# Kernel tuning notes

Measured on AMD Instinct MI355X. Metric: run time of the kernel, lower is better.

Reference implementation:

```python
import jax, jax.numpy as jnp
import numpy as np

B, L, H, C = 1, 512, 1024, 2


def setup_inputs() -> dict:
    key = jax.random.key(0)
    k1, k2, k3 = jax.random.split(key, 3)
    lm_output = jax.random.normal(k1, (B, L, H), dtype=jnp.float32)
    # torch Linear weight layout: [out_features, in_features]
    W1 = jax.random.normal(k2, (H, 2 * H), dtype=jnp.float32) * 0.02
    b1 = jnp.zeros((H,), dtype=jnp.float32)
    W2 = jax.random.normal(k3, (C, H), dtype=jnp.float32) * 0.02
    b2 = jnp.zeros((C,), dtype=jnp.float32)
    return {"lm_output": lm_output, "W1": W1, "b1": b1, "W2": W2, "b2": b2}


def reference(lm_output, W1, b1, W2, b2):
    # pair_emb[b,i,j] = concat(lm_output[b,j], lm_output[b,i])
    # Linear(concat(a,b)) decomposes: split W1 into the halves acting on each part.
    Wa = W1[:, :H]  # acts on lm_output_a (the j / column token)
    Wb = W1[:, H:]  # acts on lm_output_b (the i / row token)
    a_proj = jnp.einsum('blh,oh->blo', lm_output, Wa)  # [B,L,H]
    b_proj = jnp.einsum('blh,oh->blo', lm_output, Wb)  # [B,L,H]
    # hidden[b,i,j] = tanh(a_proj[b,j] + b_proj[b,i] + b1)   -> [B,L,L,H]
    hidden = jnp.tanh(a_proj[:, None, :, :] + b_proj[:, :, None, :] + b1)
    # Dropout is identity at inference time.
    logits = jnp.einsum('bijh,ch->bijc', hidden, W2) + b2  # [B,L,L,C]
    logits = (logits + jnp.swapaxes(logits, 1, 2)) / 2.0
    return logits
```

## Files before the change

kernel.cpp:

```cpp
#include <hip/hip_runtime.h>
#include <hip/hip_bf16.h>

#define HH 1024
#define LL 512
#define NT 16
#define NTRI 136

typedef __attribute__((ext_vector_type(8))) short bf16x8;
typedef __attribute__((ext_vector_type(4))) float f32x4;
typedef __attribute__((ext_vector_type(2))) float f32x2;

static constexpr float C_EXP = 2.8853900817779268f;

static __device__ __forceinline__ uint4 pack8(float4 a, float4 b) {
    union { uint4 u; __hip_bfloat162 h[4]; } r;
    r.h[0] = __float22bfloat162_rn(make_float2(a.x, a.y));
    r.h[1] = __float22bfloat162_rn(make_float2(a.z, a.w));
    r.h[2] = __float22bfloat162_rn(make_float2(b.x, b.y));
    r.h[3] = __float22bfloat162_rn(make_float2(b.z, b.w));
    return r.u;
}

__global__ __launch_bounds__(256) void convert_kernel(
    const float* __restrict__ lm, const float* __restrict__ W1,
    const float* __restrict__ W2,
    ushort* __restrict__ lm16, ushort* __restrict__ B16, float* __restrict__ wsum)
{
    const int b = blockIdx.x;
    if (b == 1280) {
        const int tid = threadIdx.x;
        if (tid < 128) {
            const int c = tid >> 6, l = tid & 63;
            float s = 0.f;
            for (int q = l; q < 256; q += 64) {
                const float4 v = *(const float4*)&W2[c * HH + q * 4];
                s += v.x + v.y + v.z + v.w;
            }
#pragma unroll
            for (int off = 32; off; off >>= 1) s += __shfl_down(s, off, 64);
            if (l == 0) wsum[c] = s;
        }
        return;
    }
    const int q = b * 256 + threadIdx.x;
    if (q < 65536) {
        const float4 a = *(const float4*)&lm[q * 8];
        const float4 c = *(const float4*)&lm[q * 8 + 4];
        ((uint4*)lm16)[q] = pack8(a, c);
    } else {
        const int p = q - 65536;
        const int n = p >> 7, k8 = (p & 127) * 8;
        const float* src = &W1[(n & 1023) * 2048 + (n >> 10) * 1024 + k8];
        ((uint4*)B16)[p] = pack8(*(const float4*)src, *(const float4*)(src + 4));
    }
}

__global__ __launch_bounds__(256, 4) void proj_mfma_kernel(
    const ushort* __restrict__ lm16, const ushort* __restrict__ B16,
    const float* __restrict__ b1, float* __restrict__ Ea, float* __restrict__ Eb)
{
    __shared__ ushort As[64][136];
    __shared__ ushort Bs[64][136];

    const int tid  = threadIdx.x;
    const int lane = tid & 63;
    const int w    = tid >> 6;
    const int b    = blockIdx.x;
    const int xcd  = b & 7;
    const int idx  = b >> 3;
    const int nbase = (xcd * 4 + (idx & 3)) * 64;
    const int mbase = (idx >> 2) * 64;
    const int wm   = w * 16;

    const int frow = lane & 15;
    const int q8   = (lane >> 4) * 8;

    f32x4 acc[4] = {};

    for (int kb = 0; kb < HH; kb += 128) {
        __syncthreads();
        {
            int p = tid;
#pragma unroll
            for (int it = 0; it < 4; ++it, p += 256) {
                const int row = p >> 4, c8 = (p & 15) * 8;
                *(uint4*)&As[row][c8] = *(const uint4*)&lm16[(mbase + row) * HH + kb + c8];
                *(uint4*)&Bs[row][c8] = *(const uint4*)&B16[(nbase + row) * HH + kb + c8];
            }
        }
        __syncthreads();

#pragma unroll
        for (int s = 0; s < 4; ++s) {
            const bf16x8 a = *(const bf16x8*)&As[wm + frow][s * 32 + q8];
#pragma unroll
            for (int nf = 0; nf < 4; ++nf) {
                const bf16x8 bb = *(const bf16x8*)&Bs[nf * 16 + frow][s * 32 + q8];
                acc[nf] = __builtin_amdgcn_mfma_f32_16x16x32_bf16(a, bb, acc[nf], 0, 0, 0);
            }
        }
    }

    const int col = lane & 15;
    const int rq  = (lane >> 4) * 4;
    const int m0  = mbase + wm + rq;
    const bool isA = nbase < HH;
#pragma unroll
    for (int nf = 0; nf < 4; ++nf) {
        const int nn = (nbase + nf * 16 + col) & 1023;
        if (isA) {
            const float bb = b1[nn];
#pragma unroll
            for (int r = 0; r < 4; ++r)
                Ea[(m0 + r) * HH + nn] = __builtin_amdgcn_exp2f(C_EXP * (acc[nf][r] + bb));
        } else {
#pragma unroll
            for (int r = 0; r < 4; ++r)
                Eb[(m0 + r) * HH + nn] = __builtin_amdgcn_exp2f(C_EXP * acc[nf][r]);
        }
    }
}

__global__ __launch_bounds__(256, 4) void pair_kernel(
    const float* __restrict__ Ea, const float* __restrict__ Eb,
    const float* __restrict__ W2, float* __restrict__ pbuf, int slice)
{
    __shared__ float eaj[32][68];
    __shared__ float eai[32][68];
    __shared__ float ebi[32][68];
    __shared__ float ebj[32][68];
    __shared__ f32x2 ws2[128];

    const int tid = threadIdx.x;
    const int tx  = tid & 15;
    const int ty  = tid >> 4;

    int tt = blockIdx.x, bi = 0, rem = NT;
    while (tt >= rem) { tt -= rem; --rem; ++bi; }
    const int bj    = bi + tt;
    const int ibase = bi * 32;
    const int jbase = bj * 32;
    const int k0    = blockIdx.y * slice;

    if (tid < slice)
        ws2[tid] = (f32x2){W2[k0 + tid], W2[HH + k0 + tid]};

    f32x2 acc2[2][2] = {};
    const f32x2 one2 = {1.f, 1.f};

    for (int kb = 0; kb < slice; kb += 64) {
        __syncthreads();
        {
            int p = tid;
#pragma unroll
            for (int it = 0; it < 8; ++it, p += 256) {
                const int tile = p >> 9;
                const int row  = (p >> 4) & 31;
                const int c4   = p & 15;
                float4 v;
                if      (tile == 0) v = *(const float4*)&Ea[(jbase + row) * HH + k0 + kb + c4 * 4];
                else if (tile == 1) v = *(const float4*)&Ea[(ibase + row) * HH + k0 + kb + c4 * 4];
                else if (tile == 2) v = *(const float4*)&Eb[(ibase + row) * HH + k0 + kb + c4 * 4];
                else                v = *(const float4*)&Eb[(jbase + row) * HH + k0 + kb + c4 * 4];
                if      (tile == 0) *(float4*)&eaj[row][c4 * 4] = v;
                else if (tile == 1) *(float4*)&eai[row][c4 * 4] = v;
                else if (tile == 2) *(float4*)&ebi[row][c4 * 4] = v;
                else                *(float4*)&ebj[row][c4 * 4] = v;
            }
        }
        __syncthreads();

#pragma unroll 4
        for (int h4 = 0; h4 < 16; ++h4) {
            const float4 Aj0 = *(const float4*)&eaj[tx][h4 * 4];
            const float4 Aj1 = *(const float4*)&eaj[tx + 16][h4 * 4];
            const float4 Bi0 = *(const float4*)&ebi[ty][h4 * 4];
            const float4 Bi1 = *(const float4*)&ebi[ty + 16][h4 * 4];
            const float4 Ai0 = *(const float4*)&eai[ty][h4 * 4];
            const float4 Ai1 = *(const float4*)&eai[ty + 16][h4 * 4];
            const float4 Bj0 = *(const float4*)&ebj[tx][h4 * 4];
            const float4 Bj1 = *(const float4*)&ebj[tx + 16][h4 * 4];
            const f32x4 wA = *(const f32x4*)&ws2[kb + h4 * 4];
            const f32x4 wB = *(const f32x4*)&ws2[kb + h4 * 4 + 2];

#define DO_H(AJ0v, AJ1v, BI0v, BI1v, AI0v, AI1v, BJ0v, BJ1v, W01)            \
            {                                                                 \
                const f32x2 Aj = {AJ0v, AJ1v};                                \
                const f32x2 Bj = {BJ0v, BJ1v};                                \
                const f32x2 d0 = __builtin_elementwise_fma((f32x2){BI0v, BI0v}, Aj, one2); \
                const f32x2 d1 = __builtin_elementwise_fma((f32x2){BI1v, BI1v}, Aj, one2); \
                const f32x2 e0 = __builtin_elementwise_fma((f32x2){AI0v, AI0v}, Bj, one2); \
                const f32x2 e1 = __builtin_elementwise_fma((f32x2){AI1v, AI1v}, Bj, one2); \
                const float dp0 = d0.x * d0.y, dp1 = d1.x * d1.y;             \
                const float ep0 = e0.x * e0.y, ep1 = e1.x * e1.y;             \
                const float DR = __builtin_amdgcn_rcpf(dp0 * dp1);            \
                const float ER = __builtin_amdgcn_rcpf(ep0 * ep1);            \
                const f32x2 dq = (f32x2){DR, DR} * (f32x2){dp1, dp0};         \
                const f32x2 eq = (f32x2){ER, ER} * (f32x2){ep1, ep0};         \
                const f32x2 u0 = (f32x2){dq.x, dq.x} * d0.yx + (f32x2){eq.x, eq.x} * e0.yx; \
                const f32x2 u1 = (f32x2){dq.y, dq.y} * d1.yx + (f32x2){eq.y, eq.y} * e1.yx; \
                acc2[0][0] = __builtin_elementwise_fma((f32x2){u0.x, u0.x}, (W01), acc2[0][0]); \
                acc2[0][1] = __builtin_elementwise_fma((f32x2){u0.y, u0.y}, (W01), acc2[0][1]); \
                acc2[1][0] = __builtin_elementwise_fma((f32x2){u1.x, u1.x}, (W01), acc2[1][0]); \
                acc2[1][1] = __builtin_elementwise_fma((f32x2){u1.y, u1.y}, (W01), acc2[1][1]); \
            }
            DO_H(Aj0.x, Aj1.x, Bi0.x, Bi1.x, Ai0.x, Ai1.x, Bj0.x, Bj1.x, wA.xy)
            DO_H(Aj0.y, Aj1.y, Bi0.y, Bi1.y, Ai0.y, Ai1.y, Bj0.y, Bj1.y, wA.zw)
            DO_H(Aj0.z, Aj1.z, Bi0.z, Bi1.z, Ai0.z, Ai1.z, Bj0.z, Bj1.z, wB.xy)
            DO_H(Aj0.w, Aj1.w, Bi0.w, Bi1.w, Ai0.w, Ai1.w, Bj0.w, Bj1.w, wB.zw)
#undef DO_H
        }
    }

    float* pb = pbuf + ((size_t)blockIdx.y * NTRI + blockIdx.x) * 2048;
#pragma unroll
    for (int ii = 0; ii < 2; ++ii)
#pragma unroll
        for (int jj = 0; jj < 2; ++jj) {
            const int li = ty + ii * 16, lj = tx + jj * 16;
            *(f32x2*)&pb[(li * 32 + lj) * 2] = acc2[ii][jj];
        }
}

__global__ __launch_bounds__(256) void combine_kernel(
    const float* __restrict__ pbuf, const float* __restrict__ b2,
    const float* __restrict__ wsum, float* __restrict__ out, int nz)
{
    const int idx   = blockIdx.x * 256 + threadIdx.x;
    const int t     = idx >> 11;
    const int local = idx & 2047;
    int tt = t, bi = 0, rem = NT;
    while (tt >= rem) { tt -= rem; --rem; ++bi; }
    const int bj = bi + tt;

    float s0 = 0.f, s1 = 0.f;
    for (int z = 0; z < nz; z += 2) {
        s0 += pbuf[((size_t)z * NTRI + t) * 2048 + local];
        s1 += pbuf[((size_t)(z + 1) * NTRI + t) * 2048 + local];
    }
    const float s = s0 + s1;

    const int li = local >> 6;
    const int lj = (local >> 1) & 31;
    const int c  = local & 1;
    const float v = wsum[c] + b2[c] - s;

    const int i = bi * 32 + li;
    const int j = bj * 32 + lj;
    out[(i * LL + j) * 2 + c] = v;
    out[(j * LL + i) * 2 + c] = v;
}

extern "C" void kernel_launch(void* const* d_in, const int* in_sizes, int n_in,
                              void* d_out, int out_size, void* d_ws, size_t ws_size,
                              hipStream_t stream)
{
    const float* lm = (const float*)d_in[0];
    const float* W1 = (const float*)d_in[1];
    const float* b1 = (const float*)d_in[2];
    const float* W2 = (const float*)d_in[3];
    const float* b2 = (const float*)d_in[4];
    float* out = (float*)d_out;

    char* ws = (char*)d_ws;
    float*  Ea   = (float*)ws;
    float*  Eb   = (float*)(ws + (2u << 20));
    float*  wsum = (float*)(ws + (4u << 20));
    char*   ub   = ws + (4u << 20) + 256;
    ushort* lm16 = (ushort*)ub;
    ushort* B16  = (ushort*)(ub + (1u << 20));
    float*  pbuf = (float*)ub;

    const size_t ubase  = (4u << 20) + 256;
    const size_t pb16   = (size_t)16 * NTRI * 2048 * 4;
    const int nz = (ws_size >= ubase + pb16) ? 16 : 8;
    const int slice = HH / nz;

    convert_kernel<<<1281, 256, 0, stream>>>(lm, W1, W2, lm16, B16, wsum);
    proj_mfma_kernel<<<256, 256, 0, stream>>>(lm16, B16, b1, Ea, Eb);
    pair_kernel<<<dim3(NTRI, nz), 256, 0, stream>>>(Ea, Eb, W2, pbuf, slice);
    combine_kernel<<<(NTRI * 2048) / 256, 256, 0, stream>>>(pbuf, b2, wsum, out, nz);
}
```

Measured before the change: 129.5 us.

## Fuse combine into pair kernel via last-block atomic counter reduction

Removes the separate combine kernel launch. Each pair block now increments a per-tile atomic counter after writing its partial sums, and the last of the nz slice blocks for a tile reduces all partials and writes both symmetric output entries. Counters are zeroed in the convert kernel and the workspace layout shifts to make room for them. This saves a launch and its gap, but the final reduction is serialized onto whichever block finishes last for each tile, and it adds fences and atomics.

```diff
diff --git a/kernel.cpp b/kernel.cpp
--- a/kernel.cpp
+++ b/kernel.cpp
@@ -24,7 +24,8 @@
 __global__ __launch_bounds__(256) void convert_kernel(
     const float* __restrict__ lm, const float* __restrict__ W1,
     const float* __restrict__ W2,
-    ushort* __restrict__ lm16, ushort* __restrict__ B16, float* __restrict__ wsum)
+    ushort* __restrict__ lm16, ushort* __restrict__ B16,
+    float* __restrict__ wsum, uint* __restrict__ cnt)
 {
     const int b = blockIdx.x;
     if (b == 1280) {
@@ -40,6 +41,7 @@
             for (int off = 32; off; off >>= 1) s += __shfl_down(s, off, 64);
             if (l == 0) wsum[c] = s;
         }
+        if (tid < NTRI) cnt[tid] = 0;
         return;
     }
     const int q = b * 256 + threadIdx.x;
@@ -123,13 +125,16 @@
 
 __global__ __launch_bounds__(256, 4) void pair_kernel(
     const float* __restrict__ Ea, const float* __restrict__ Eb,
-    const float* __restrict__ W2, float* __restrict__ pbuf, int slice)
+    const float* __restrict__ W2, const float* __restrict__ b2,
+    const float* __restrict__ wsum, float* __restrict__ pbuf,
+    uint* __restrict__ cnt, float* __restrict__ out, int slice, int nz)
 {
     __shared__ float eaj[32][68];
     __shared__ float eai[32][68];
     __shared__ float ebi[32][68];
     __shared__ float ebj[32][68];
     __shared__ f32x2 ws2[128];
+    __shared__ int  s_last;
 
     const int tid = threadIdx.x;
     const int tx  = tid & 15;
@@ -220,35 +225,35 @@
             const int li = ty + ii * 16, lj = tx + jj * 16;
             *(f32x2*)&pb[(li * 32 + lj) * 2] = acc2[ii][jj];
         }
-}
-
-__global__ __launch_bounds__(256) void combine_kernel(
-    const float* __restrict__ pbuf, const float* __restrict__ b2,
-    const float* __restrict__ wsum, float* __restrict__ out, int nz)
-{
-    const int idx   = blockIdx.x * 256 + threadIdx.x;
-    const int t     = idx >> 11;
-    const int local = idx & 2047;
-    int tt = t, bi = 0, rem = NT;
-    while (tt >= rem) { tt -= rem; --rem; ++bi; }
-    const int bj = bi + tt;
-
-    float s0 = 0.f, s1 = 0.f;
-    for (int z = 0; z < nz; z += 2) {
-        s0 += pbuf[((size_t)z * NTRI + t) * 2048 + local];
-        s1 += pbuf[((size_t)(z + 1) * NTRI + t) * 2048 + local];
-    }
-    const float s = s0 + s1;
-
-    const int li = local >> 6;
-    const int lj = (local >> 1) & 31;
-    const int c  = local & 1;
-    const float v = wsum[c] + b2[c] - s;
-
-    const int i = bi * 32 + li;
-    const int j = bj * 32 + lj;
-    out[(i * LL + j) * 2 + c] = v;
-    out[(j * LL + i) * 2 + c] = v;
+
+    __threadfence();
+    if (tid == 0) {
+        const uint old = atomicAdd(&cnt[blockIdx.x], 1u);
+        s_last = (old == (uint)(nz - 1));
+    }
+    __syncthreads();
+    if (!s_last) return;
+    __threadfence();
+
+    const float base0 = wsum[0] + b2[0];
+    const float base1 = wsum[1] + b2[1];
+#pragma unroll
+    for (int k = 0; k < 8; ++k) {
+        const int local = k * 256 + tid;
+        float s0 = 0.f, s1 = 0.f;
+        for (int z = 0; z < nz; z += 2) {
+            s0 += pbuf[((size_t)z * NTRI + blockIdx.x) * 2048 + local];
+            s1 += pbuf[((size_t)(z + 1) * NTRI + blockIdx.x) * 2048 + local];
+        }
+        const int li = local >> 6;
+        const int lj = (local >> 1) & 31;
+        const int c  = local & 1;
+        const float v = (c ? base1 : base0) - (s0 + s1);
+        const int i = ibase + li;
+        const int j = jbase + lj;
+        out[(i * LL + j) * 2 + c] = v;
+        out[(j * LL + i) * 2 + c] = v;
+    }
 }
 
 extern "C" void kernel_launch(void* const* d_in, const int* in_sizes, int n_in,
@@ -266,18 +271,19 @@
     float*  Ea   = (float*)ws;
     float*  Eb   = (float*)(ws + (2u << 20));
     float*  wsum = (float*)(ws + (4u << 20));
-    char*   ub   = ws + (4u << 20) + 256;
+    uint*   cnt  = (uint*) (ws + (4u << 20) + 64);
+    char*   ub   = ws + (4u << 20) + 1024;
     ushort* lm16 = (ushort*)ub;
     ushort* B16  = (ushort*)(ub + (1u << 20));
     float*  pbuf = (float*)ub;
 
-    const size_t ubase  = (4u << 20) + 256;
+    const size_t ubase  = (4u << 20) + 1024;
     const size_t pb16   = (size_t)16 * NTRI * 2048 * 4;
     const int nz = (ws_size >= ubase + pb16) ? 16 : 8;
     const int slice = HH / nz;
 
-    convert_kernel<<<1281, 256, 0, stream>>>(lm, W1, W2, lm16, B16, wsum);
+    convert_kernel<<<1281, 256, 0, stream>>>(lm, W1, W2, lm16, B16, wsum, cnt);
     proj_mfma_kernel<<<256, 256, 0, stream>>>(lm16, B16, b1, Ea, Eb);
-    pair_kernel<<<dim3(NTRI, nz), 256, 0, stream>>>(Ea, Eb, W2, pbuf, slice);
-    combine_kernel<<<(NTRI * 2048) / 256, 256, 0, stream>>>(pbuf, b2, wsum, out, nz);
-}
+    pair_kernel<<<dim3(NTRI, nz), 256, 0, stream>>>(Ea, Eb, W2, b2, wsum,
+                                                    pbuf, cnt, out, slice, nz);
+}
```

Result: slower. 338.6 us (+161.5%).

## Fuse bf16 conversion into projection GEMM and W2-sum into combine kernel

Applied to the files above, without the earlier changes.

Drops the separate conversion kernel. The projection GEMM now reads fp32 lm and W1 directly, packs them to bf16 while staging into shared memory, and handles the W1 half split through its own indexing. The W2 row-sum plus b2 is now computed per block inside the combine kernel, which removes one launch and the bf16 intermediate buffers. In exchange, every GEMM tile reads twice as many bytes from global memory, the same fp32 data is re-read and re-converted by several blocks, and each combine block repeats a small reduction.

```diff
diff --git a/kernel.cpp b/kernel.cpp
--- a/kernel.cpp
+++ b/kernel.cpp
@@ -21,42 +21,8 @@
     return r.u;
 }
 
-__global__ __launch_bounds__(256) void convert_kernel(
+__global__ __launch_bounds__(256, 4) void proj_mfma_kernel(
     const float* __restrict__ lm, const float* __restrict__ W1,
-    const float* __restrict__ W2,
-    ushort* __restrict__ lm16, ushort* __restrict__ B16, float* __restrict__ wsum)
-{
-    const int b = blockIdx.x;
-    if (b == 1280) {
-        const int tid = threadIdx.x;
-        if (tid < 128) {
-            const int c = tid >> 6, l = tid & 63;
-            float s = 0.f;
-            for (int q = l; q < 256; q += 64) {
-                const float4 v = *(const float4*)&W2[c * HH + q * 4];
-                s += v.x + v.y + v.z + v.w;
-            }
-#pragma unroll
-            for (int off = 32; off; off >>= 1) s += __shfl_down(s, off, 64);
-            if (l == 0) wsum[c] = s;
-        }
-        return;
-    }
-    const int q = b * 256 + threadIdx.x;
-    if (q < 65536) {
-        const float4 a = *(const float4*)&lm[q * 8];
-        const float4 c = *(const float4*)&lm[q * 8 + 4];
-        ((uint4*)lm16)[q] = pack8(a, c);
-    } else {
-        const int p = q - 65536;
-        const int n = p >> 7, k8 = (p & 127) * 8;
-        const float* src = &W1[(n & 1023) * 2048 + (n >> 10) * 1024 + k8];
-        ((uint4*)B16)[p] = pack8(*(const float4*)src, *(const float4*)(src + 4));
-    }
-}
-
-__global__ __launch_bounds__(256, 4) void proj_mfma_kernel(
-    const ushort* __restrict__ lm16, const ushort* __restrict__ B16,
     const float* __restrict__ b1, float* __restrict__ Ea, float* __restrict__ Eb)
 {
     __shared__ ushort As[64][136];
@@ -71,6 +37,8 @@
     const int nbase = (xcd * 4 + (idx & 3)) * 64;
     const int mbase = (idx >> 2) * 64;
     const int wm   = w * 16;
+    const int sel  = nbase >> 10;
+    const int nrow = nbase & 1023;
 
     const int frow = lane & 15;
     const int q8   = (lane >> 4) * 8;
@@ -84,8 +52,10 @@
 #pragma unroll
             for (int it = 0; it < 4; ++it, p += 256) {
                 const int row = p >> 4, c8 = (p & 15) * 8;
-                *(uint4*)&As[row][c8] = *(const uint4*)&lm16[(mbase + row) * HH + kb + c8];
-                *(uint4*)&Bs[row][c8] = *(const uint4*)&B16[(nbase + row) * HH + kb + c8];
+                const float* pa = &lm[(mbase + row) * HH + kb + c8];
+                *(uint4*)&As[row][c8] = pack8(*(const float4*)pa, *(const float4*)(pa + 4));
+                const float* pw = &W1[(nrow + row) * 2048 + sel * 1024 + kb + c8];
+                *(uint4*)&Bs[row][c8] = pack8(*(const float4*)pw, *(const float4*)(pw + 4));
             }
         }
         __syncthreads();
@@ -104,10 +74,10 @@
     const int col = lane & 15;
     const int rq  = (lane >> 4) * 4;
     const int m0  = mbase + wm + rq;
-    const bool isA = nbase < HH;
+    const bool isA = sel == 0;
 #pragma unroll
     for (int nf = 0; nf < 4; ++nf) {
-        const int nn = (nbase + nf * 16 + col) & 1023;
+        const int nn = (nrow + nf * 16 + col);
         if (isA) {
             const float bb = b1[nn];
 #pragma unroll
@@ -223,10 +193,27 @@
 }
 
 __global__ __launch_bounds__(256) void combine_kernel(
-    const float* __restrict__ pbuf, const float* __restrict__ b2,
-    const float* __restrict__ wsum, float* __restrict__ out, int nz)
-{
-    const int idx   = blockIdx.x * 256 + threadIdx.x;
+    const float* __restrict__ pbuf, const float* __restrict__ W2,
+    const float* __restrict__ b2, float* __restrict__ out, int nz)
+{
+    __shared__ float s_ws[2];
+
+    const int tid = threadIdx.x;
+    if (tid < 128) {
+        const int c = tid >> 6, l = tid & 63;
+        float s = 0.f;
+#pragma unroll
+        for (int q = 0; q < 4; ++q) {
+            const float4 v = *(const float4*)&W2[c * HH + (l + q * 64) * 4];
+            s += v.x + v.y + v.z + v.w;
+        }
+#pragma unroll
+        for (int off = 32; off; off >>= 1) s += __shfl_down(s, off, 64);
+        if (l == 0) s_ws[c] = s + b2[c];
+    }
+    __syncthreads();
+
+    const int idx   = blockIdx.x * 256 + tid;
     const int t     = idx >> 11;
     const int local = idx & 2047;
     int tt = t, bi = 0, rem = NT;
@@ -243,7 +230,7 @@
     const int li = local >> 6;
     const int lj = (local >> 1) & 31;
     const int c  = local & 1;
-    const float v = wsum[c] + b2[c] - s;
+    const float v = s_ws[c] - s;
 
     const int i = bi * 32 + li;
     const int j = bj * 32 + lj;
@@ -263,21 +250,16 @@
     float* out = (float*)d_out;
 
     char* ws = (char*)d_ws;
-    float*  Ea   = (float*)ws;
-    float*  Eb   = (float*)(ws + (2u << 20));
-    float*  wsum = (float*)(ws + (4u << 20));
-    char*   ub   = ws + (4u << 20) + 256;
-    ushort* lm16 = (ushort*)ub;
-    ushort* B16  = (ushort*)(ub + (1u << 20));
-    float*  pbuf = (float*)ub;
-
-    const size_t ubase  = (4u << 20) + 256;
-    const size_t pb16   = (size_t)16 * NTRI * 2048 * 4;
+    float* Ea   = (float*)ws;
+    float* Eb   = (float*)(ws + (2u << 20));
+    float* pbuf = (float*)(ws + (4u << 20) + 64);
+
+    const size_t ubase = (4u << 20) + 64;
+    const size_t pb16  = (size_t)16 * NTRI * 2048 * 4;
     const int nz = (ws_size >= ubase + pb16) ? 16 : 8;
     const int slice = HH / nz;
 
-    convert_kernel<<<1281, 256, 0, stream>>>(lm, W1, W2, lm16, B16, wsum);
-    proj_mfma_kernel<<<256, 256, 0, stream>>>(lm16, B16, b1, Ea, Eb);
+    proj_mfma_kernel<<<256, 256, 0, stream>>>(lm, W1, b1, Ea, Eb);
     pair_kernel<<<dim3(NTRI, nz), 256, 0, stream>>>(Ea, Eb, W2, pbuf, slice);
-    combine_kernel<<<(NTRI * 2048) / 256, 256, 0, stream>>>(pbuf, b2, wsum, out, nz);
-}
+    combine_kernel<<<(NTRI * 2048) / 256, 256, 0, stream>>>(pbuf, W2, b2, out, nz);
+}
```

Result: no change. 129.4 us (-0.0%).
